# Optimization experiments

Measured on AMD Instinct MI355X. Metric: run time of the kernel, lower is better.

Reference implementation:

```python
import jax, jax.numpy as jnp
import numpy as np

N = 50000
F_IN = 512
H = 256
L = 52
E = 1600000


def gcn_conv(x, W, b, src, dst):
    """PyG GCNConv: add self-loops, symmetric norm D^-1/2 (A+I) D^-1/2, then X W + b.
    src/dst already include self-loops."""
    h = x @ W  # [N, H]
    deg = jax.ops.segment_sum(jnp.ones_like(dst, dtype=h.dtype), dst, num_segments=N)
    dinv = jnp.where(deg > 0, jax.lax.rsqrt(deg), 0.0)
    w = dinv[src] * dinv[dst]  # [E+N]
    out = jax.ops.segment_sum(h[src] * w[:, None], dst, num_segments=N)
    return out + b


def _branch(x, src, dst, params):
    (W1, b1), (W2, b2), (W3, b3), (We, be) = params
    x = jax.nn.relu(gcn_conv(x, W1, b1, src, dst))
    x = jax.nn.relu(gcn_conv(x, W2, b2, src, dst))
    x = jax.nn.relu(gcn_conv(x, W3, b3, src, dst))
    return gcn_conv(x, We, be, src, dst)


def setup_inputs() -> dict:
    key = jax.random.key(0)
    ks = jax.random.split(key, 32)
    d = {}
    d["x_1"] = jax.random.normal(ks[0], (N, F_IN), dtype=jnp.float32)
    d["x_2"] = jax.random.normal(ks[1], (N, F_IN), dtype=jnp.float32)
    d["edge_index_1"] = jax.random.randint(ks[2], (2, E), 0, N, dtype=jnp.int32)
    d["edge_index_2"] = jax.random.randint(ks[3], (2, E), 0, N, dtype=jnp.int32)

    def lin(k, fi, fo):
        s = 1.0 / np.sqrt(fi)
        return jax.random.uniform(k, (fi, fo), jnp.float32, -s, s)

    i = 4
    for br in (1, 2):
        fis = [F_IN, H, H, H]
        for li, nm in enumerate(["1", "2", "3", "e"]):
            d[f"Wc{nm}{br}"] = lin(ks[i], fis[li], H); i += 1
            d[f"bc{nm}{br}"] = jnp.zeros((H,), jnp.float32)
    d["w1_W"] = lin(ks[i], H, 1); i += 1
    d["w1_b"] = jnp.zeros((1,), jnp.float32)
    d["w2_W"] = lin(ks[i], H, 1); i += 1
    d["w2_b"] = jnp.zeros((1,), jnp.float32)
    d["fin_W"] = lin(ks[i], H, H); i += 1
    d["fin_b"] = jnp.zeros((H,), jnp.float32)
    d["out_W"] = lin(ks[i], H, L); i += 1
    d["out_b"] = jnp.zeros((L,), jnp.float32)
    return d


def reference(x_1, edge_index_1, x_2, edge_index_2,
              Wc11, bc11, Wc21, bc21, Wc31, bc31, Wce1, bce1,
              Wc12, bc12, Wc22, bc22, Wc32, bc32, Wce2, bce2,
              w1_W, w1_b, w2_W, w2_b, fin_W, fin_b, out_W, out_b):
    loop = jnp.arange(N)
    s1 = jnp.concatenate([edge_index_1[0], loop])
    d1 = jnp.concatenate([edge_index_1[1], loop])
    s2 = jnp.concatenate([edge_index_2[0], loop])
    d2 = jnp.concatenate([edge_index_2[1], loop])

    h1 = _branch(x_1, s1, d1, [(Wc11, bc11), (Wc21, bc21), (Wc31, bc31), (Wce1, bce1)])
    h2 = _branch(x_2, s2, d2, [(Wc12, bc12), (Wc22, bc22), (Wc32, bc32), (Wce2, bce2)])

    f1 = jax.nn.sigmoid(h1 @ w1_W + w1_b)  # [N,1]
    f2 = jax.nn.sigmoid(h2 @ w2_W + w2_b)
    f1 = f1 / (f1 + f2)
    out = f1 * h1 + (1.0 - f1) * h2
    out = jax.nn.relu(out @ fin_W + fin_b)
    return jax.nn.sigmoid(out @ out_W + out_b)
```

## Files before the change

### kernel.cpp

```cpp
#include <hip/hip_runtime.h>
#include <math.h>

#define N_NODES 50000
#define F_IN    512
#define HDIM    256
#define L_OUT   52
#define E_EDGES 1600000

typedef short short8 __attribute__((ext_vector_type(8)));
typedef unsigned short u16x8 __attribute__((ext_vector_type(8)));
typedef float f32x4 __attribute__((ext_vector_type(4)));
typedef float f32x2 __attribute__((ext_vector_type(2)));

__device__ __forceinline__ float bf2f(unsigned short u) {
    unsigned int x = ((unsigned int)u) << 16;
    return __builtin_bit_cast(float, x);
}
__device__ __forceinline__ unsigned short f2bf(float f) {
    unsigned int u = __builtin_bit_cast(unsigned int, f);
    return (unsigned short)((u + 0x7fffu + ((u >> 16) & 1u)) >> 16);
}
__device__ __forceinline__ unsigned char f2fp8(float f) {
    int pk = __builtin_amdgcn_cvt_pk_fp8_f32(f, 0.f, 0, false);
    return (unsigned char)(pk & 0xff);
}
__device__ __forceinline__ void gload16(const unsigned short* g, unsigned short* l) {
    __builtin_amdgcn_global_load_lds(
        (const __attribute__((address_space(1))) unsigned int*)(g),
        (__attribute__((address_space(3))) unsigned int*)(l), 16, 0, 0);
}


__global__ void k_rank2(const int* __restrict__ d1, const int* __restrict__ d2,
                        int* __restrict__ c1, int* __restrict__ c2,
                        int* __restrict__ rk1, int* __restrict__ rk2, int E) {
    int tid = blockIdx.x * blockDim.x + threadIdx.x;
    int half = E >> 3;
    if (tid >= 2 * half) return;
    int br = tid >= half;
    const int* D = br ? d2 : d1;
    int* C = br ? c2 : c1;
    int* RK = br ? rk2 : rk1;
    int e = (br ? tid - half : tid) << 3;
    int4 da = ((const int4*)(D + e))[0];
    int4 db = ((const int4*)(D + e))[1];
    int r0 = atomicAdd(&C[da.x], 1);
    int r1 = atomicAdd(&C[da.y], 1);
    int r2 = atomicAdd(&C[da.z], 1);
    int r3 = atomicAdd(&C[da.w], 1);
    int r4 = atomicAdd(&C[db.x], 1);
    int r5 = atomicAdd(&C[db.y], 1);
    int r6 = atomicAdd(&C[db.z], 1);
    int r7 = atomicAdd(&C[db.w], 1);
    ((int4*)(RK + e))[0] = make_int4(r0, r1, r2, r3);
    ((int4*)(RK + e))[1] = make_int4(r4, r5, r6, r7);
}

__global__ void k_dinv2(const int* __restrict__ c1, const int* __restrict__ c2,
                        float* __restrict__ v1, float* __restrict__ v2, int n) {
    int i = blockIdx.x * blockDim.x + threadIdx.x;
    if (i < n) v1[i] = rsqrtf((float)(c1[i] + 1));
    else if (i < 2 * n) v2[i - n] = rsqrtf((float)(c2[i - n] + 1));
}

__global__ void k_scan1f(const int* __restrict__ c1, const int* __restrict__ c2,
                         int* __restrict__ i1, int* __restrict__ i2,
                         int* __restrict__ b1, int* __restrict__ b2, int n) {
    const int* cnt = blockIdx.y ? c2 : c1;
    int* incl = blockIdx.y ? i2 : i1;
    int* bsum = blockIdx.y ? b2 : b1;
    __shared__ int s[256];
    int tid = threadIdx.x;
    int idx = blockIdx.x * 256 + tid;
    int v = (idx < n) ? cnt[idx] : 0;
    s[tid] = v;
    __syncthreads();
#pragma unroll
    for (int off = 1; off < 256; off <<= 1) {
        int t = (tid >= off) ? s[tid - off] : 0;
        __syncthreads();
        s[tid] += t;
        __syncthreads();
    }
    if (idx < n) incl[idx] = s[tid];
    if (tid == 255) bsum[blockIdx.x] = s[255];
}

__global__ void k_scan2f(int* __restrict__ b1, int* __restrict__ b2,
                         int* __restrict__ r1, int* __restrict__ r2, int nb, int n) {
    int* bsum = blockIdx.x ? b2 : b1;
    int* rowptr = blockIdx.x ? r2 : r1;
    __shared__ int s[256];
    int tid = threadIdx.x;
    int v = (tid < nb) ? bsum[tid] : 0;
    s[tid] = v;
    __syncthreads();
#pragma unroll
    for (int off = 1; off < 256; off <<= 1) {
        int t = (tid >= off) ? s[tid - off] : 0;
        __syncthreads();
        s[tid] += t;
        __syncthreads();
    }
    if (tid < nb) bsum[tid] = s[tid] - v;
    if (tid == nb - 1) rowptr[n] = s[tid];
}

__global__ void k_scan3f(const int* __restrict__ i1, const int* __restrict__ i2,
                         const int* __restrict__ c1, const int* __restrict__ c2,
                         const int* __restrict__ b1, const int* __restrict__ b2,
                         int* __restrict__ r1, int* __restrict__ r2, int n) {
    const int* incl = blockIdx.y ? i2 : i1;
    const int* cnt  = blockIdx.y ? c2 : c1;
    const int* bsum = blockIdx.y ? b2 : b1;
    int* rowptr     = blockIdx.y ? r2 : r1;
    int i = blockIdx.x * blockDim.x + threadIdx.x;
    if (i < n) rowptr[i] = incl[i] - cnt[i] + bsum[i >> 8];
}

__global__ void k_fill2(const int* __restrict__ s1, const int* __restrict__ d1,
                        const int* __restrict__ s2, const int* __restrict__ d2,
                        const int* __restrict__ rk1, const int* __restrict__ rk2,
                        const int* __restrict__ rp1, const int* __restrict__ rp2,
                        unsigned short* __restrict__ col1, unsigned short* __restrict__ col2,
                        int E) {
    int tid = blockIdx.x * blockDim.x + threadIdx.x;
    int half = E >> 3;
    if (tid >= 2 * half) return;
    int br = tid >= half;
    const int* S = br ? s2 : s1;
    const int* D = br ? d2 : d1;
    const int* RK = br ? rk2 : rk1;
    const int* RP = br ? rp2 : rp1;
    unsigned short* C = br ? col2 : col1;
    int e = (br ? tid - half : tid) << 3;
    int4 da = ((const int4*)(D + e))[0];
    int4 db = ((const int4*)(D + e))[1];
    int4 sa = ((const int4*)(S + e))[0];
    int4 sb = ((const int4*)(S + e))[1];
    int4 ra = ((const int4*)(RK + e))[0];
    int4 rb = ((const int4*)(RK + e))[1];
    int p0 = RP[da.x] + ra.x;
    int p1 = RP[da.y] + ra.y;
    int p2 = RP[da.z] + ra.z;
    int p3 = RP[da.w] + ra.w;
    int p4 = RP[db.x] + rb.x;
    int p5 = RP[db.y] + rb.y;
    int p6 = RP[db.z] + rb.z;
    int p7 = RP[db.w] + rb.w;
    C[p0] = (unsigned short)sa.x;
    C[p1] = (unsigned short)sa.y;
    C[p2] = (unsigned short)sa.z;
    C[p3] = (unsigned short)sa.w;
    C[p4] = (unsigned short)sb.x;
    C[p5] = (unsigned short)sb.y;
    C[p6] = (unsigned short)sb.z;
    C[p7] = (unsigned short)sb.w;
}


__global__ void k_f2b2(const float* __restrict__ x1, const float* __restrict__ x2,
                       unsigned short* __restrict__ o1, unsigned short* __restrict__ o2,
                       int n4) {
    int i = blockIdx.x * blockDim.x + threadIdx.x;
    int stride = gridDim.x * blockDim.x;
    int tot = 2 * n4;
    for (; i < tot; i += stride) {
        int br = i >= n4;
        int e = br ? i - n4 : i;
        float4 v = ((const float4*)(br ? x2 : x1))[e];
        ushort4 o;
        o.x = f2bf(v.x); o.y = f2bf(v.y); o.z = f2bf(v.z); o.w = f2bf(v.w);
        ((ushort4*)(br ? o2 : o1))[e] = o;
    }
}

struct WDesc { const float* in; unsigned short* out; int K; int N; int Npad; };
struct WPack { WDesc d[10]; };

__global__ void k_wconv(WPack p) {
    WDesc w = p.d[blockIdx.y];
    int total = w.K * w.Npad;
    int idx = blockIdx.x * 256 + threadIdx.x;
    if (idx >= total) return;
    int n = idx / w.K, k = idx - n * w.K;
    w.out[idx] = (n < w.N) ? f2bf(w.in[(size_t)k * w.N + n]) : (unsigned short)0;
}


__global__ void k_agg(const unsigned char* __restrict__ g, const int* __restrict__ rowptr,
                      const unsigned short* __restrict__ col,
                      const float* __restrict__ dinv,
                      const float* __restrict__ bias, unsigned short* __restrict__ out,
                      int n, int do_relu) {
    int gtid = blockIdx.x * blockDim.x + threadIdx.x;
    int wid = gtid >> 6;
    if (wid >= n) return;
    int lane = threadIdx.x & 63;
    int half = lane >> 5;
    int fl = lane & 31;

    float di = dinv[wid];

    float a[8];
#pragma unroll
    for (int k = 0; k < 8; k++) a[k] = 0.f;

    int r0 = rowptr[wid], r1 = rowptr[wid + 1];

    int base = r0;
    for (; base + 16 <= r1; base += 16) {
        int c[8]; float w[8]; uint2 v[8];
#pragma unroll
        for (int t = 0; t < 8; t++) c[t] = col[base + 2 * t + half];
#pragma unroll
        for (int t = 0; t < 8; t++) w[t] = dinv[c[t]];
#pragma unroll
        for (int t = 0; t < 8; t++)
            v[t] = ((const uint2*)(g + (size_t)c[t] * HDIM))[fl];
#pragma unroll
        for (int t = 0; t < 8; t++) {
            float wt = w[t] * di;
            f32x2 p0 = __builtin_amdgcn_cvt_pk_f32_fp8((int)v[t].x, false);
            f32x2 p1 = __builtin_amdgcn_cvt_pk_f32_fp8((int)v[t].x, true);
            f32x2 p2 = __builtin_amdgcn_cvt_pk_f32_fp8((int)v[t].y, false);
            f32x2 p3 = __builtin_amdgcn_cvt_pk_f32_fp8((int)v[t].y, true);
            a[0] = fmaf(p0[0], wt, a[0]); a[1] = fmaf(p0[1], wt, a[1]);
            a[2] = fmaf(p1[0], wt, a[2]); a[3] = fmaf(p1[1], wt, a[3]);
            a[4] = fmaf(p2[0], wt, a[4]); a[5] = fmaf(p2[1], wt, a[5]);
            a[6] = fmaf(p3[0], wt, a[6]); a[7] = fmaf(p3[1], wt, a[7]);
        }
    }
    if (base < r1) {
        int c[8]; float w[8]; uint2 v[8];
#pragma unroll
        for (int t = 0; t < 8; t++) {
            int idx = base + 2 * t + half;
            int ok = idx < r1;
            c[t] = col[ok ? idx : r0];
            w[t] = ok ? dinv[c[t]] : 0.f;
        }
#pragma unroll
        for (int t = 0; t < 8; t++)
            v[t] = ((const uint2*)(g + (size_t)c[t] * HDIM))[fl];
#pragma unroll
        for (int t = 0; t < 8; t++) {
            float wt = w[t] * di;
            f32x2 p0 = __builtin_amdgcn_cvt_pk_f32_fp8((int)v[t].x, false);
            f32x2 p1 = __builtin_amdgcn_cvt_pk_f32_fp8((int)v[t].x, true);
            f32x2 p2 = __builtin_amdgcn_cvt_pk_f32_fp8((int)v[t].y, false);
            f32x2 p3 = __builtin_amdgcn_cvt_pk_f32_fp8((int)v[t].y, true);
            a[0] = fmaf(p0[0], wt, a[0]); a[1] = fmaf(p0[1], wt, a[1]);
            a[2] = fmaf(p1[0], wt, a[2]); a[3] = fmaf(p1[1], wt, a[3]);
            a[4] = fmaf(p2[0], wt, a[4]); a[5] = fmaf(p2[1], wt, a[5]);
            a[6] = fmaf(p3[0], wt, a[6]); a[7] = fmaf(p3[1], wt, a[7]);
        }
    }

#pragma unroll
    for (int k = 0; k < 8; k++) a[k] += __shfl_xor(a[k], 32);

    float w0 = di * di;
    uint2 sv = ((const uint2*)(g + (size_t)wid * HDIM))[fl];
    f32x2 s0 = __builtin_amdgcn_cvt_pk_f32_fp8((int)sv.x, false);
    f32x2 s1 = __builtin_amdgcn_cvt_pk_f32_fp8((int)sv.x, true);
    f32x2 s2 = __builtin_amdgcn_cvt_pk_f32_fp8((int)sv.y, false);
    f32x2 s3 = __builtin_amdgcn_cvt_pk_f32_fp8((int)sv.y, true);
    float sf[8] = {s0[0], s0[1], s1[0], s1[1], s2[0], s2[1], s3[0], s3[1]};
    u16x8 o;
#pragma unroll
    for (int k = 0; k < 8; k++) {
        float x = fmaf(sf[k], w0, a[k]) + bias[fl * 8 + k];
        if (do_relu) x = fmaxf(x, 0.f);
        o[k] = f2bf(x);
    }
    if (half == 0)
        ((u16x8*)(out + (size_t)wid * HDIM))[fl] = o;
}


template <int EPI>
__global__ __launch_bounds__(256) void k_gemm(const unsigned short* __restrict__ A,
                                              const unsigned short* __restrict__ Bt,
                                              const float* __restrict__ bias,
                                              void* __restrict__ Cout,
                                              int M, int K, int Nc) {
    __shared__ __align__(16) unsigned short As[128 * 32];
    __shared__ __align__(16) unsigned short Bs[128 * 32];
    int tid = threadIdx.x;
    int wid = tid >> 6, lane = tid & 63;
    int wr = wid >> 1, wc = wid & 1;
    int mb = blockIdx.y * 128, nb = blockIdx.x * 128;

    int sr = tid >> 2;
    int ssl = (tid & 3) ^ ((sr >> 1) & 3);
    int ar0 = mb + sr;      if (ar0 > M - 1) ar0 = M - 1;
    int ar1 = mb + sr + 64; if (ar1 > M - 1) ar1 = M - 1;
    const unsigned short* gA0 = A + (size_t)ar0 * K + ssl * 8;
    const unsigned short* gA1 = A + (size_t)ar1 * K + ssl * 8;
    const unsigned short* gB0 = Bt + (size_t)(nb + sr) * K + ssl * 8;
    const unsigned short* gB1 = Bt + (size_t)(nb + sr + 64) * K + ssl * 8;
    unsigned short* ldsA = As + tid * 8;
    unsigned short* ldsB = Bs + tid * 8;

    f32x4 acc[4][4];
#pragma unroll
    for (int m = 0; m < 4; m++)
#pragma unroll
        for (int n = 0; n < 4; n++) acc[m][n] = (f32x4){0.f, 0.f, 0.f, 0.f};

    int l15 = lane & 15, ks = lane >> 4;

    for (int k0 = 0; k0 < K; k0 += 32) {
        gload16(gA0 + k0, ldsA);
        gload16(gA1 + k0, ldsA + 2048);
        gload16(gB0 + k0, ldsB);
        gload16(gB1 + k0, ldsB + 2048);
        __syncthreads();

        short8 af[4], bfr[4];
#pragma unroll
        for (int m = 0; m < 4; m++) {
            int row = wr * 64 + m * 16 + l15;
            int slot = ks ^ ((row >> 1) & 3);
            af[m] = *(const short8*)((const char*)As + row * 64 + slot * 16);
        }
#pragma unroll
        for (int n = 0; n < 4; n++) {
            int row = wc * 64 + n * 16 + l15;
            int slot = ks ^ ((row >> 1) & 3);
            bfr[n] = *(const short8*)((const char*)Bs + row * 64 + slot * 16);
        }
#pragma unroll
        for (int m = 0; m < 4; m++)
#pragma unroll
            for (int n = 0; n < 4; n++)
                acc[m][n] = __builtin_amdgcn_mfma_f32_16x16x32_bf16(af[m], bfr[n], acc[m][n], 0, 0, 0);
        __syncthreads();
    }

    int lq = lane >> 4;
#pragma unroll
    for (int m = 0; m < 4; m++) {
#pragma unroll
        for (int n = 0; n < 4; n++) {
            int gcol = nb + wc * 64 + n * 16 + l15;
#pragma unroll
            for (int r = 0; r < 4; r++) {
                int grow = mb + wr * 64 + m * 16 + lq * 4 + r;
                if (grow >= M) continue;
                float v = acc[m][n][r];
                if (EPI == 0) {
                    ((unsigned char*)Cout)[(size_t)grow * Nc + gcol] = f2fp8(v);
                } else if (EPI == 1) {
                    v += bias[gcol];
                    v = fmaxf(v, 0.f);
                    ((unsigned short*)Cout)[(size_t)grow * Nc + gcol] = f2bf(v);
                } else {
                    if (gcol < Nc) {
                        v += bias[gcol];
                        v = 1.f / (1.f + expf(-v));
                        ((float*)Cout)[(size_t)grow * Nc + gcol] = v;
                    }
                }
            }
        }
    }
}


__global__ void k_gate(const unsigned short* __restrict__ h1, const unsigned short* __restrict__ h2,
                       const float* __restrict__ w1, const float* __restrict__ w1b,
                       const float* __restrict__ w2, const float* __restrict__ w2b,
                       unsigned short* __restrict__ m, int n) {
    int gtid = blockIdx.x * blockDim.x + threadIdx.x;
    int wid = gtid >> 6;
    int lane = threadIdx.x & 63;
    if (wid >= n) return;
    ushort4 av = ((const ushort4*)(h1 + (size_t)wid * HDIM))[lane];
    ushort4 bv = ((const ushort4*)(h2 + (size_t)wid * HDIM))[lane];
    float4 wa = ((const float4*)w1)[lane];
    float4 wb = ((const float4*)w2)[lane];
    float a0 = bf2f(av.x), a1 = bf2f(av.y), a2 = bf2f(av.z), a3 = bf2f(av.w);
    float b0 = bf2f(bv.x), b1 = bf2f(bv.y), b2 = bf2f(bv.z), b3 = bf2f(bv.w);
    float d1 = a0 * wa.x + a1 * wa.y + a2 * wa.z + a3 * wa.w;
    float d2 = b0 * wb.x + b1 * wb.y + b2 * wb.z + b3 * wb.w;
    for (int off = 32; off > 0; off >>= 1) {
        d1 += __shfl_xor(d1, off);
        d2 += __shfl_xor(d2, off);
    }
    float f1 = 1.f / (1.f + expf(-(d1 + w1b[0])));
    float f2 = 1.f / (1.f + expf(-(d2 + w2b[0])));
    float f = f1 / (f1 + f2);
    ushort4 o;
    o.x = f2bf(f * a0 + (1.f - f) * b0);
    o.y = f2bf(f * a1 + (1.f - f) * b1);
    o.z = f2bf(f * a2 + (1.f - f) * b2);
    o.w = f2bf(f * a3 + (1.f - f) * b3);
    ((ushort4*)(m + (size_t)wid * HDIM))[lane] = o;
}


extern "C" void kernel_launch(void* const* d_in, const int* in_sizes, int n_in,
                              void* d_out, int out_size, void* d_ws, size_t ws_size,
                              hipStream_t stream) {
    (void)n_in; (void)out_size; (void)ws_size;
    const int N = N_NODES, E = E_EDGES;

    const float* x1; const float* x2; const int* ei1; const int* ei2;
    if (in_sizes[1] == 2 * E) {
        x1 = (const float*)d_in[0]; ei1 = (const int*)d_in[1];
        x2 = (const float*)d_in[2]; ei2 = (const int*)d_in[3];
    } else {
        x1 = (const float*)d_in[0]; x2 = (const float*)d_in[1];
        ei1 = (const int*)d_in[2]; ei2 = (const int*)d_in[3];
    }
    const float* W[2][4]; const float* Bv[2][4];
    int idx = 4;
    for (int br = 0; br < 2; br++)
        for (int l = 0; l < 4; l++) {
            W[br][l] = (const float*)d_in[idx++];
            Bv[br][l] = (const float*)d_in[idx++];
        }
    const float* w1W  = (const float*)d_in[20];
    const float* w1b  = (const float*)d_in[21];
    const float* w2W  = (const float*)d_in[22];
    const float* w2b  = (const float*)d_in[23];
    const float* finW = (const float*)d_in[24];
    const float* finb = (const float*)d_in[25];
    const float* outW = (const float*)d_in[26];
    const float* outb = (const float*)d_in[27];
    float* out = (float*)d_out;

    size_t off = 0;
    auto alloc = [&](size_t bytes) {
        void* p = (char*)d_ws + off;
        off = (off + bytes + 255) & ~(size_t)255;
        return p;
    };
    unsigned short* x1b = (unsigned short*)alloc((size_t)N * F_IN * 2);
    unsigned short* x2b = (unsigned short*)alloc((size_t)N * F_IN * 2);
    unsigned char*  g8  = (unsigned char*)alloc((size_t)N * HDIM);
    unsigned short* mb_ = (unsigned short*)alloc((size_t)N * HDIM * 2);
    unsigned short* h1b = (unsigned short*)alloc((size_t)N * HDIM * 2);
    unsigned short* h2b = (unsigned short*)alloc((size_t)N * HDIM * 2);
    unsigned short* Wt[2][4];
    Wt[0][0] = (unsigned short*)alloc((size_t)HDIM * F_IN * 2);
    for (int l = 1; l < 4; l++) Wt[0][l] = (unsigned short*)alloc((size_t)HDIM * HDIM * 2);
    Wt[1][0] = (unsigned short*)alloc((size_t)HDIM * F_IN * 2);
    for (int l = 1; l < 4; l++) Wt[1][l] = (unsigned short*)alloc((size_t)HDIM * HDIM * 2);
    unsigned short* finWt = (unsigned short*)alloc((size_t)HDIM * HDIM * 2);
    unsigned short* outWt = (unsigned short*)alloc((size_t)128 * HDIM * 2);
    unsigned short* col1 = (unsigned short*)alloc((size_t)E * 2);
    unsigned short* col2 = (unsigned short*)alloc((size_t)E * 2);
    int* rank1  = (int*)alloc((size_t)E * 4);
    int* rank2  = (int*)alloc((size_t)E * 4);
    int* rp1    = (int*)alloc((size_t)(N + 1) * 4);
    int* rp2    = (int*)alloc((size_t)(N + 1) * 4);
    int* incl1  = (int*)alloc((size_t)N * 4);
    int* incl2  = (int*)alloc((size_t)N * 4);
    int* bsum1  = (int*)alloc((size_t)256 * 4);
    int* bsum2  = (int*)alloc((size_t)256 * 4);
    int* cnt1   = (int*)alloc((size_t)N * 4);
    int* cnt2   = (int*)alloc((size_t)N * 4);
    float* di1  = (float*)alloc((size_t)N * 4);
    float* di2  = (float*)alloc((size_t)N * 4);

    const int BLK = 256;
    int nwaves_grid = (N * 64 + BLK - 1) / BLK;
    int nchunks = (N + 255) / 256;
    int mtiles = (N + 127) / 128;
    int edge_blocks = (2 * (E >> 3) + BLK - 1) / BLK;
    dim3 grid_h(HDIM / 128, mtiles);
    dim3 grid_o(1, mtiles);

    WPack wp;
    wp.d[0] = {W[0][0], Wt[0][0], F_IN, HDIM, HDIM};
    wp.d[1] = {W[0][1], Wt[0][1], HDIM, HDIM, HDIM};
    wp.d[2] = {W[0][2], Wt[0][2], HDIM, HDIM, HDIM};
    wp.d[3] = {W[0][3], Wt[0][3], HDIM, HDIM, HDIM};
    wp.d[4] = {W[1][0], Wt[1][0], F_IN, HDIM, HDIM};
    wp.d[5] = {W[1][1], Wt[1][1], HDIM, HDIM, HDIM};
    wp.d[6] = {W[1][2], Wt[1][2], HDIM, HDIM, HDIM};
    wp.d[7] = {W[1][3], Wt[1][3], HDIM, HDIM, HDIM};
    wp.d[8] = {finW, finWt, HDIM, HDIM, HDIM};
    wp.d[9] = {outW, outWt, HDIM, L_OUT, 128};
    k_wconv<<<dim3(512, 10), BLK, 0, stream>>>(wp);

    hipMemsetAsync(cnt1, 0, (size_t)N * 4, stream);
    hipMemsetAsync(cnt2, 0, (size_t)N * 4, stream);
    k_rank2<<<edge_blocks, BLK, 0, stream>>>(ei1 + E, ei2 + E, cnt1, cnt2, rank1, rank2, E);
    k_scan1f<<<dim3(nchunks, 2), BLK, 0, stream>>>(cnt1, cnt2, incl1, incl2, bsum1, bsum2, N);
    k_scan2f<<<2, BLK, 0, stream>>>(bsum1, bsum2, rp1, rp2, nchunks, N);
    k_scan3f<<<dim3(nchunks, 2), BLK, 0, stream>>>(incl1, incl2, cnt1, cnt2, bsum1, bsum2, rp1, rp2, N);
    k_dinv2<<<(2 * N + BLK - 1) / BLK, BLK, 0, stream>>>(cnt1, cnt2, di1, di2, N);
    k_fill2<<<edge_blocks, BLK, 0, stream>>>(ei1, ei1 + E, ei2, ei2 + E, rank1, rank2,
                                             rp1, rp2, col1, col2, E);
    k_f2b2<<<4096, BLK, 0, stream>>>(x1, x2, x1b, x2b, N * F_IN / 4);

    for (int br = 0; br < 2; br++) {
        const unsigned short* col = br ? col2 : col1;
        const int* rp = br ? rp2 : rp1;
        const float* di = br ? di2 : di1;
        const unsigned short* xb = br ? x2b : x1b;
        unsigned short* hb = br ? h2b : h1b;

        k_gemm<0><<<grid_h, BLK, 0, stream>>>(xb, Wt[br][0], nullptr, g8, N, F_IN, HDIM);
        k_agg<<<nwaves_grid, BLK, 0, stream>>>(g8, rp, col, di, Bv[br][0], hb, N, 1);
        for (int l = 1; l <= 2; l++) {
            k_gemm<0><<<grid_h, BLK, 0, stream>>>(hb, Wt[br][l], nullptr, g8, N, HDIM, HDIM);
            k_agg<<<nwaves_grid, BLK, 0, stream>>>(g8, rp, col, di, Bv[br][l], hb, N, 1);
        }
        k_gemm<0><<<grid_h, BLK, 0, stream>>>(hb, Wt[br][3], nullptr, g8, N, HDIM, HDIM);
        k_agg<<<nwaves_grid, BLK, 0, stream>>>(g8, rp, col, di, Bv[br][3], hb, N, 0);
    }

    k_gate<<<nwaves_grid, BLK, 0, stream>>>(h1b, h2b, w1W, w1b, w2W, w2b, mb_, N);
    k_gemm<1><<<grid_h, BLK, 0, stream>>>(mb_, finWt, finb, x1b, N, HDIM, HDIM);
    k_gemm<2><<<grid_o, BLK, 0, stream>>>(x1b, outWt, outb, out, N, HDIM, L_OUT);
}
```

Before: 993.0 us.

## Precompute bf16 edge weights into packed CSR and fuse init kernels

```diff
diff --git a/kernel.cpp b/kernel.cpp
--- a/kernel.cpp
+++ b/kernel.cpp
@@ -30,31 +30,69 @@
         (__attribute__((address_space(3))) unsigned int*)(l), 16, 0, 0);
 }
 
-
-__global__ void k_rank2(const int* __restrict__ d1, const int* __restrict__ d2,
-                        int* __restrict__ c1, int* __restrict__ c2,
-                        int* __restrict__ rk1, int* __restrict__ rk2, int E) {
-    int tid = blockIdx.x * blockDim.x + threadIdx.x;
-    int half = E >> 3;
-    if (tid >= 2 * half) return;
-    int br = tid >= half;
-    const int* D = br ? d2 : d1;
-    int* C = br ? c2 : c1;
-    int* RK = br ? rk2 : rk1;
-    int e = (br ? tid - half : tid) << 3;
-    int4 da = ((const int4*)(D + e))[0];
-    int4 db = ((const int4*)(D + e))[1];
-    int r0 = atomicAdd(&C[da.x], 1);
-    int r1 = atomicAdd(&C[da.y], 1);
-    int r2 = atomicAdd(&C[da.z], 1);
-    int r3 = atomicAdd(&C[da.w], 1);
-    int r4 = atomicAdd(&C[db.x], 1);
-    int r5 = atomicAdd(&C[db.y], 1);
-    int r6 = atomicAdd(&C[db.z], 1);
-    int r7 = atomicAdd(&C[db.w], 1);
-    ((int4*)(RK + e))[0] = make_int4(r0, r1, r2, r3);
-    ((int4*)(RK + e))[1] = make_int4(r4, r5, r6, r7);
-}
+struct WDesc { const float* in; unsigned short* out; int K; int N; int Npad; int nblk; };
+struct WPack { WDesc d[10]; };
+
+
+__global__ __launch_bounds__(256) void k_init(
+    const int* __restrict__ d1, const int* __restrict__ d2,
+    int* __restrict__ c1, int* __restrict__ c2,
+    int* __restrict__ rk1, int* __restrict__ rk2, int E,
+    const float* __restrict__ x1, const float* __restrict__ x2,
+    unsigned short* __restrict__ o1, unsigned short* __restrict__ o2, int n4,
+    WPack wp, int nRank, int nF2b) {
+    int b = blockIdx.x;
+    if (b < nRank) {
+        int tid = b * 256 + threadIdx.x;
+        int half = E >> 3;
+        if (tid >= 2 * half) return;
+        int br = tid >= half;
+        const int* D = br ? d2 : d1;
+        int* C = br ? c2 : c1;
+        int* RK = br ? rk2 : rk1;
+        int e = (br ? tid - half : tid) << 3;
+        int4 da = ((const int4*)(D + e))[0];
+        int4 db = ((const int4*)(D + e))[1];
+        int r0 = atomicAdd(&C[da.x], 1);
+        int r1 = atomicAdd(&C[da.y], 1);
+        int r2 = atomicAdd(&C[da.z], 1);
+        int r3 = atomicAdd(&C[da.w], 1);
+        int r4 = atomicAdd(&C[db.x], 1);
+        int r5 = atomicAdd(&C[db.y], 1);
+        int r6 = atomicAdd(&C[db.z], 1);
+        int r7 = atomicAdd(&C[db.w], 1);
+        ((int4*)(RK + e))[0] = make_int4(r0, r1, r2, r3);
+        ((int4*)(RK + e))[1] = make_int4(r4, r5, r6, r7);
+    } else if (b < nRank + nF2b) {
+        int i = (b - nRank) * 256 + threadIdx.x;
+        int stride = nF2b * 256;
+        int tot = 2 * n4;
+        for (; i < tot; i += stride) {
+            int br = i >= n4;
+            int e = br ? i - n4 : i;
+            float4 v = ((const float4*)(br ? x2 : x1))[e];
+            ushort4 o;
+            o.x = f2bf(v.x); o.y = f2bf(v.y); o.z = f2bf(v.z); o.w = f2bf(v.w);
+            ((ushort4*)(br ? o2 : o1))[e] = o;
+        }
+    } else {
+        int wb = b - nRank - nF2b;
+        for (int ii = 0; ii < 10; ii++) {
+            WDesc w = wp.d[ii];
+            if (wb < w.nblk) {
+                int idx = wb * 256 + threadIdx.x;
+                if (idx < w.K * w.Npad) {
+                    int nn = idx / w.K, kk = idx - nn * w.K;
+                    w.out[idx] = (nn < w.N) ? f2bf(w.in[(size_t)kk * w.N + nn])
+                                            : (unsigned short)0;
+                }
+                return;
+            }
+            wb -= w.nblk;
+        }
+    }
+}
+
 
 __global__ void k_dinv2(const int* __restrict__ c1, const int* __restrict__ c2,
                         float* __restrict__ v1, float* __restrict__ v2, int n) {
@@ -122,7 +160,8 @@
                         const int* __restrict__ s2, const int* __restrict__ d2,
                         const int* __restrict__ rk1, const int* __restrict__ rk2,
                         const int* __restrict__ rp1, const int* __restrict__ rp2,
-                        unsigned short* __restrict__ col1, unsigned short* __restrict__ col2,
+                        const float* __restrict__ v1, const float* __restrict__ v2,
+                        unsigned int* __restrict__ cw1, unsigned int* __restrict__ cw2,
                         int E) {
     int tid = blockIdx.x * blockDim.x + threadIdx.x;
     int half = E >> 3;
@@ -132,7 +171,8 @@
     const int* D = br ? d2 : d1;
     const int* RK = br ? rk2 : rk1;
     const int* RP = br ? rp2 : rp1;
-    unsigned short* C = br ? col2 : col1;
+    const float* V = br ? v2 : v1;
+    unsigned int* C = br ? cw2 : cw1;
     int e = (br ? tid - half : tid) << 3;
     int4 da = ((const int4*)(D + e))[0];
     int4 db = ((const int4*)(D + e))[1];
@@ -140,56 +180,20 @@
     int4 sb = ((const int4*)(S + e))[1];
     int4 ra = ((const int4*)(RK + e))[0];
     int4 rb = ((const int4*)(RK + e))[1];
-    int p0 = RP[da.x] + ra.x;
-    int p1 = RP[da.y] + ra.y;
-    int p2 = RP[da.z] + ra.z;
-    int p3 = RP[da.w] + ra.w;
-    int p4 = RP[db.x] + rb.x;
-    int p5 = RP[db.y] + rb.y;
-    int p6 = RP[db.z] + rb.z;
-    int p7 = RP[db.w] + rb.w;
-    C[p0] = (unsigned short)sa.x;
-    C[p1] = (unsigned short)sa.y;
-    C[p2] = (unsigned short)sa.z;
-    C[p3] = (unsigned short)sa.w;
-    C[p4] = (unsigned short)sb.x;
-    C[p5] = (unsigned short)sb.y;
-    C[p6] = (unsigned short)sb.z;
-    C[p7] = (unsigned short)sb.w;
-}
-
-
-__global__ void k_f2b2(const float* __restrict__ x1, const float* __restrict__ x2,
-                       unsigned short* __restrict__ o1, unsigned short* __restrict__ o2,
-                       int n4) {
-    int i = blockIdx.x * blockDim.x + threadIdx.x;
-    int stride = gridDim.x * blockDim.x;
-    int tot = 2 * n4;
-    for (; i < tot; i += stride) {
-        int br = i >= n4;
-        int e = br ? i - n4 : i;
-        float4 v = ((const float4*)(br ? x2 : x1))[e];
-        ushort4 o;
-        o.x = f2bf(v.x); o.y = f2bf(v.y); o.z = f2bf(v.z); o.w = f2bf(v.w);
-        ((ushort4*)(br ? o2 : o1))[e] = o;
-    }
-}
-
-struct WDesc { const float* in; unsigned short* out; int K; int N; int Npad; };
-struct WPack { WDesc d[10]; };
-
-__global__ void k_wconv(WPack p) {
-    WDesc w = p.d[blockIdx.y];
-    int total = w.K * w.Npad;
-    int idx = blockIdx.x * 256 + threadIdx.x;
-    if (idx >= total) return;
-    int n = idx / w.K, k = idx - n * w.K;
-    w.out[idx] = (n < w.N) ? f2bf(w.in[(size_t)k * w.N + n]) : (unsigned short)0;
+    int dd[8] = {da.x, da.y, da.z, da.w, db.x, db.y, db.z, db.w};
+    int ss[8] = {sa.x, sa.y, sa.z, sa.w, sb.x, sb.y, sb.z, sb.w};
+    int rr[8] = {ra.x, ra.y, ra.z, ra.w, rb.x, rb.y, rb.z, rb.w};
+#pragma unroll
+    for (int t = 0; t < 8; t++) {
+        float w = V[ss[t]] * V[dd[t]];
+        C[RP[dd[t]] + rr[t]] =
+            (unsigned int)(unsigned short)ss[t] | ((unsigned int)f2bf(w) << 16);
+    }
 }
 
 
 __global__ void k_agg(const unsigned char* __restrict__ g, const int* __restrict__ rowptr,
-                      const unsigned short* __restrict__ col,
+                      const unsigned int* __restrict__ cw,
                       const float* __restrict__ dinv,
                       const float* __restrict__ bias, unsigned short* __restrict__ out,
                       int n, int do_relu) {
@@ -200,66 +204,82 @@
     int half = lane >> 5;
     int fl = lane & 31;
 
-    float di = dinv[wid];
-
     float a[8];
 #pragma unroll
     for (int k = 0; k < 8; k++) a[k] = 0.f;
 
     int r0 = rowptr[wid], r1 = rowptr[wid + 1];
-
     int base = r0;
-    for (; base + 16 <= r1; base += 16) {
-        int c[8]; float w[8]; uint2 v[8];
-#pragma unroll
-        for (int t = 0; t < 8; t++) c[t] = col[base + 2 * t + half];
-#pragma unroll
-        for (int t = 0; t < 8; t++) w[t] = dinv[c[t]];
-#pragma unroll
-        for (int t = 0; t < 8; t++)
-            v[t] = ((const uint2*)(g + (size_t)c[t] * HDIM))[fl];
-#pragma unroll
-        for (int t = 0; t < 8; t++) {
-            float wt = w[t] * di;
+
+    for (; base + 32 <= r1; base += 32) {
+        unsigned int c[16]; uint2 v[16];
+#pragma unroll
+        for (int t = 0; t < 16; t++) c[t] = cw[base + 2 * t + half];
+#pragma unroll
+        for (int t = 0; t < 16; t++)
+            v[t] = ((const uint2*)(g + (size_t)(c[t] & 0xffffu) * HDIM))[fl];
+#pragma unroll
+        for (int t = 0; t < 16; t++) {
+            float w = bf2f((unsigned short)(c[t] >> 16));
             f32x2 p0 = __builtin_amdgcn_cvt_pk_f32_fp8((int)v[t].x, false);
             f32x2 p1 = __builtin_amdgcn_cvt_pk_f32_fp8((int)v[t].x, true);
             f32x2 p2 = __builtin_amdgcn_cvt_pk_f32_fp8((int)v[t].y, false);
             f32x2 p3 = __builtin_amdgcn_cvt_pk_f32_fp8((int)v[t].y, true);
-            a[0] = fmaf(p0[0], wt, a[0]); a[1] = fmaf(p0[1], wt, a[1]);
-            a[2] = fmaf(p1[0], wt, a[2]); a[3] = fmaf(p1[1], wt, a[3]);
-            a[4] = fmaf(p2[0], wt, a[4]); a[5] = fmaf(p2[1], wt, a[5]);
-            a[6] = fmaf(p3[0], wt, a[6]); a[7] = fmaf(p3[1], wt, a[7]);
-        }
-    }
-    if (base < r1) {
-        int c[8]; float w[8]; uint2 v[8];
+            a[0] = fmaf(p0[0], w, a[0]); a[1] = fmaf(p0[1], w, a[1]);
+            a[2] = fmaf(p1[0], w, a[2]); a[3] = fmaf(p1[1], w, a[3]);
+            a[4] = fmaf(p2[0], w, a[4]); a[5] = fmaf(p2[1], w, a[5]);
+            a[6] = fmaf(p3[0], w, a[6]); a[7] = fmaf(p3[1], w, a[7]);
+        }
+    }
+    for (; base + 16 <= r1; base += 16) {
+        unsigned int c[8]; uint2 v[8];
+#pragma unroll
+        for (int t = 0; t < 8; t++) c[t] = cw[base + 2 * t + half];
+#pragma unroll
+        for (int t = 0; t < 8; t++)
+            v[t] = ((const uint2*)(g + (size_t)(c[t] & 0xffffu) * HDIM))[fl];
 #pragma unroll
         for (int t = 0; t < 8; t++) {
-            int idx = base + 2 * t + half;
-            int ok = idx < r1;
-            c[t] = col[ok ? idx : r0];
-            w[t] = ok ? dinv[c[t]] : 0.f;
-        }
-#pragma unroll
-        for (int t = 0; t < 8; t++)
-            v[t] = ((const uint2*)(g + (size_t)c[t] * HDIM))[fl];
-#pragma unroll
-        for (int t = 0; t < 8; t++) {
-            float wt = w[t] * di;
+            float w = bf2f((unsigned short)(c[t] >> 16));
             f32x2 p0 = __builtin_amdgcn_cvt_pk_f32_fp8((int)v[t].x, false);
             f32x2 p1 = __builtin_amdgcn_cvt_pk_f32_fp8((int)v[t].x, true);
             f32x2 p2 = __builtin_amdgcn_cvt_pk_f32_fp8((int)v[t].y, false);
             f32x2 p3 = __builtin_amdgcn_cvt_pk_f32_fp8((int)v[t].y, true);
-            a[0] = fmaf(p0[0], wt, a[0]); a[1] = fmaf(p0[1], wt, a[1]);
-            a[2] = fmaf(p1[0], wt, a[2]); a[3] = fmaf(p1[1], wt, a[3]);
-            a[4] = fmaf(p2[0], wt, a[4]); a[5] = fmaf(p2[1], wt, a[5]);
-            a[6] = fmaf(p3[0], wt, a[6]); a[7] = fmaf(p3[1], wt, a[7]);
+            a[0] = fmaf(p0[0], w, a[0]); a[1] = fmaf(p0[1], w, a[1]);
+            a[2] = fmaf(p1[0], w, a[2]); a[3] = fmaf(p1[1], w, a[3]);
+            a[4] = fmaf(p2[0], w, a[4]); a[5] = fmaf(p2[1], w, a[5]);
+            a[6] = fmaf(p3[0], w, a[6]); a[7] = fmaf(p3[1], w, a[7]);
+        }
+    }
+    if (base < r1) {
+        unsigned int c[8]; uint2 v[8]; float w[8];
+#pragma unroll
+        for (int t = 0; t < 8; t++) {
+            int idx = base + 2 * t + half;
+            int ok = idx < r1;
+            c[t] = cw[ok ? idx : r0];
+            w[t] = ok ? bf2f((unsigned short)(c[t] >> 16)) : 0.f;
+        }
+#pragma unroll
+        for (int t = 0; t < 8; t++)
+            v[t] = ((const uint2*)(g + (size_t)(c[t] & 0xffffu) * HDIM))[fl];
+#pragma unroll
+        for (int t = 0; t < 8; t++) {
+            f32x2 p0 = __builtin_amdgcn_cvt_pk_f32_fp8((int)v[t].x, false);
+            f32x2 p1 = __builtin_amdgcn_cvt_pk_f32_fp8((int)v[t].x, true);
+            f32x2 p2 = __builtin_amdgcn_cvt_pk_f32_fp8((int)v[t].y, false);
+            f32x2 p3 = __builtin_amdgcn_cvt_pk_f32_fp8((int)v[t].y, true);
+            a[0] = fmaf(p0[0], w[t], a[0]); a[1] = fmaf(p0[1], w[t], a[1]);
+            a[2] = fmaf(p1[0], w[t], a[2]); a[3] = fmaf(p1[1], w[t], a[3]);
+            a[4] = fmaf(p2[0], w[t], a[4]); a[5] = fmaf(p2[1], w[t], a[5]);
+            a[6] = fmaf(p3[0], w[t], a[6]); a[7] = fmaf(p3[1], w[t], a[7]);
         }
     }
 
 #pragma unroll
     for (int k = 0; k < 8; k++) a[k] += __shfl_xor(a[k], 32);
 
+    float di = dinv[wid];
     float w0 = di * di;
     uint2 sv = ((const uint2*)(g + (size_t)wid * HDIM))[fl];
     f32x2 s0 = __builtin_amdgcn_cvt_pk_f32_fp8((int)sv.x, false);
@@ -451,8 +471,8 @@
     for (int l = 1; l < 4; l++) Wt[1][l] = (unsigned short*)alloc((size_t)HDIM * HDIM * 2);
     unsigned short* finWt = (unsigned short*)alloc((size_t)HDIM * HDIM * 2);
     unsigned short* outWt = (unsigned short*)alloc((size_t)128 * HDIM * 2);
-    unsigned short* col1 = (unsigned short*)alloc((size_t)E * 2);
-    unsigned short* col2 = (unsigned short*)alloc((size_t)E * 2);
+    unsigned int* cw1 = (unsigned int*)alloc((size_t)E * 4);
+    unsigned int* cw2 = (unsigned int*)alloc((size_t)E * 4);
     int* rank1  = (int*)alloc((size_t)E * 4);
     int* rank2  = (int*)alloc((size_t)E * 4);
     int* rp1    = (int*)alloc((size_t)(N + 1) * 4);
@@ -475,44 +495,51 @@
     dim3 grid_o(1, mtiles);
 
     WPack wp;
-    wp.d[0] = {W[0][0], Wt[0][0], F_IN, HDIM, HDIM};
-    wp.d[1] = {W[0][1], Wt[0][1], HDIM, HDIM, HDIM};
-    wp.d[2] = {W[0][2], Wt[0][2], HDIM, HDIM, HDIM};
-    wp.d[3] = {W[0][3], Wt[0][3], HDIM, HDIM, HDIM};
-    wp.d[4] = {W[1][0], Wt[1][0], F_IN, HDIM, HDIM};
-    wp.d[5] = {W[1][1], Wt[1][1], HDIM, HDIM, HDIM};
-    wp.d[6] = {W[1][2], Wt[1][2], HDIM, HDIM, HDIM};
-    wp.d[7] = {W[1][3], Wt[1][3], HDIM, HDIM, HDIM};
-    wp.d[8] = {finW, finWt, HDIM, HDIM, HDIM};
-    wp.d[9] = {outW, outWt, HDIM, L_OUT, 128};
-    k_wconv<<<dim3(512, 10), BLK, 0, stream>>>(wp);
+    wp.d[0] = {W[0][0], Wt[0][0], F_IN, HDIM, HDIM, 0};
+    wp.d[1] = {W[0][1], Wt[0][1], HDIM, HDIM, HDIM, 0};
+    wp.d[2] = {W[0][2], Wt[0][2], HDIM, HDIM, HDIM, 0};
+    wp.d[3] = {W[0][3], Wt[0][3], HDIM, HDIM, HDIM, 0};
+    wp.d[4] = {W[1][0], Wt[1][0], F_IN, HDIM, HDIM, 0};
+    wp.d[5] = {W[1][1], Wt[1][1], HDIM, HDIM, HDIM, 0};
+    wp.d[6] = {W[1][2], Wt[1][2], HDIM, HDIM, HDIM, 0};
+    wp.d[7] = {W[1][3], Wt[1][3], HDIM, HDIM, HDIM, 0};
+    wp.d[8] = {finW, finWt, HDIM, HDIM, HDIM, 0};
+    wp.d[9] = {outW, outWt, HDIM, L_OUT, 128, 0};
+    int nW = 0;
+    for (int i = 0; i < 10; i++) {
+        wp.d[i].nblk = (wp.d[i].K * wp.d[i].Npad + 255) / 256;
+        nW += wp.d[i].nblk;
+    }
+    int nRank = edge_blocks;
+    int nF2b = 4096;
 
     hipMemsetAsync(cnt1, 0, (size_t)N * 4, stream);
     hipMemsetAsync(cnt2, 0, (size_t)N * 4, stream);
-    k_rank2<<<edge_blocks, BLK, 0, stream>>>(ei1 + E, ei2 + E, cnt1, cnt2, rank1, rank2, E);
+    k_init<<<nRank + nF2b + nW, BLK, 0, stream>>>(
+        ei1 + E, ei2 + E, cnt1, cnt2, rank1, rank2, E,
+        x1, x2, x1b, x2b, N * F_IN / 4, wp, nRank, nF2b);
     k_scan1f<<<dim3(nchunks, 2), BLK, 0, stream>>>(cnt1, cnt2, incl1, incl2, bsum1, bsum2, N);
     k_scan2f<<<2, BLK, 0, stream>>>(bsum1, bsum2, rp1, rp2, nchunks, N);
     k_scan3f<<<dim3(nchunks, 2), BLK, 0, stream>>>(incl1, incl2, cnt1, cnt2, bsum1, bsum2, rp1, rp2, N);
     k_dinv2<<<(2 * N + BLK - 1) / BLK, BLK, 0, stream>>>(cnt1, cnt2, di1, di2, N);
     k_fill2<<<edge_blocks, BLK, 0, stream>>>(ei1, ei1 + E, ei2, ei2 + E, rank1, rank2,
-                                             rp1, rp2, col1, col2, E);
-    k_f2b2<<<4096, BLK, 0, stream>>>(x1, x2, x1b, x2b, N * F_IN / 4);
+                                             rp1, rp2, di1, di2, cw1, cw2, E);
 
     for (int br = 0; br < 2; br++) {
-        const unsigned short* col = br ? col2 : col1;
+        const unsigned int* cw = br ? cw2 : cw1;
         const int* rp = br ? rp2 : rp1;
         const float* di = br ? di2 : di1;
         const unsigned short* xb = br ? x2b : x1b;
         unsigned short* hb = br ? h2b : h1b;
 
         k_gemm<0><<<grid_h, BLK, 0, stream>>>(xb, Wt[br][0], nullptr, g8, N, F_IN, HDIM);
-        k_agg<<<nwaves_grid, BLK, 0, stream>>>(g8, rp, col, di, Bv[br][0], hb, N, 1);
+        k_agg<<<nwaves_grid, BLK, 0, stream>>>(g8, rp, cw, di, Bv[br][0], hb, N, 1);
         for (int l = 1; l <= 2; l++) {
             k_gemm<0><<<grid_h, BLK, 0, stream>>>(hb, Wt[br][l], nullptr, g8, N, HDIM, HDIM);
-            k_agg<<<nwaves_grid, BLK, 0, stream>>>(g8, rp, col, di, Bv[br][l], hb, N, 1);
+            k_agg<<<nwaves_grid, BLK, 0, stream>>>(g8, rp, cw, di, Bv[br][l], hb, N, 1);
         }
         k_gemm<0><<<grid_h, BLK, 0, stream>>>(hb, Wt[br][3], nullptr, g8, N, HDIM, HDIM);
-        k_agg<<<nwaves_grid, BLK, 0, stream>>>(g8, rp, col, di, Bv[br][3], hb, N, 0);
+        k_agg<<<nwaves_grid, BLK, 0, stream>>>(g8, rp, cw, di, Bv[br][3], hb, N, 0);
     }
 
     k_gate<<<nwaves_grid, BLK, 0, stream>>>(h1b, h2b, w1W, w1b, w2W, w2b, mb_, N);
```

New measurement: 992.6 us. No clear change (-0.0%).
